# Optimization experiments

Measured on AMD Instinct MI355X. Metric: run time of the kernel, lower is better.

## Reference

```python
import jax, jax.numpy as jnp
import numpy as np

D = 128      # flattened state dim (n_dim)
T = 128      # time grid length
N = 32       # quadrature nodes per integral
H = 256      # func MLP hidden
HK = 64      # kernel MLP hidden
ITERS = 3    # IDESolver max_iterations


def setup_inputs() -> dict:
    key = jax.random.key(0)
    ks = jax.random.split(key, 6)
    z0 = jax.random.normal(ks[0], (1, D), jnp.float32)
    t = jnp.linspace(0.0, 1.0, T, dtype=jnp.float32)
    W1 = jax.random.normal(ks[1], (D, H), jnp.float32) / np.float32(np.sqrt(D))
    b1 = jnp.zeros((H,), jnp.float32)
    W2 = jax.random.normal(ks[2], (H, D), jnp.float32) / np.float32(np.sqrt(H))
    b2 = jnp.zeros((D,), jnp.float32)
    Wk1 = jax.random.normal(ks[3], (2, HK), jnp.float32) / np.float32(np.sqrt(2))
    bk1 = jnp.zeros((HK,), jnp.float32)
    # small kernel init keeps the Picard iteration stable
    Wk2 = jax.random.normal(ks[4], (HK, D * D), jnp.float32) * np.float32(0.01 / np.sqrt(HK))
    bk2 = jnp.zeros((D * D,), jnp.float32)
    return dict(z0=z0, t=t, W1=W1, b1=b1, W2=W2, b2=b2,
                Wk1=Wk1, bk1=bk1, Wk2=Wk2, bk2=bk2)


def _spline_coeffs(x, y):
    # natural cubic spline second derivatives M: tridiagonal system, natural BC
    n = x.shape[0]
    h = x[1:] - x[:-1]                       # [T-1]
    A = jnp.zeros((n, n), y.dtype).at[0, 0].set(1.0).at[n - 1, n - 1].set(1.0)
    idx = jnp.arange(1, n - 1)
    A = A.at[idx, idx - 1].set(h[:-1])
    A = A.at[idx, idx].set(2.0 * (h[:-1] + h[1:]))
    A = A.at[idx, idx + 1].set(h[1:])
    slope = (y[1:] - y[:-1]) / h[:, None]
    rhs = jnp.zeros_like(y).at[1:-1].set(6.0 * (slope[1:] - slope[:-1]))
    return jnp.linalg.solve(A, rhs)          # [T, D]


def _spline_eval(x, y, M, q):
    # evaluate spline at flat query points q [Q] -> [Q, D]
    qc = jnp.clip(q, x[0], x[-1])
    i = jnp.clip(jnp.searchsorted(x, qc, side='right') - 1, 0, x.shape[0] - 2)
    h = x[i + 1] - x[i]
    a = (x[i + 1] - qc) / h
    b = (qc - x[i]) / h
    return (a[:, None] * y[i] + b[:, None] * y[i + 1]
            + ((a ** 3 - a)[:, None] * M[i] + (b ** 3 - b)[:, None] * M[i + 1])
            * (h ** 2 / 6.0)[:, None])


def _F(y, W1, b1, W2, b2):
    return jnp.tanh(y @ W1 + b1) @ W2 + b2


def _K(ts, Wk1, bk1, Wk2, bk2):
    # ts [..., 2] -> kernel matrices [..., D, D]
    hden = jnp.tanh(ts @ Wk1 + bk1)
    return (hden @ Wk2 + bk2).reshape(ts.shape[:-1] + (D, D))


def reference(z0, t, W1, b1, W2, b2, Wk1, bk1, Wk2, bk2):
    y0 = z0.reshape(-1)                          # solver state: flattened z0 [D]
    u = jnp.linspace(0.0, 1.0, N, dtype=t.dtype) # unit quad nodes
    wq = jnp.ones((N,), t.dtype).at[0].set(0.5).at[-1].set(0.5)  # trapezoid
    mids = 0.5 * (t[:-1] + t[1:])
    xs = jnp.concatenate([t, mids])              # eval points [P = 2T-1]
    hstep = t[1:] - t[:-1]
    yg = jnp.broadcast_to(y0, (T, D))            # Picard initial guess y^(0)=y0
    for _ in range(ITERS):
        M = _spline_coeffs(t, yg)
        s = xs[:, None] * u[None, :]                              # [P, N], lb=0, ub=x
        ys = _spline_eval(t, yg, M, s.reshape(-1)).reshape(-1, N, D)
        fy = _F(ys, W1, b1, W2, b2)                               # [P, N, D]
        ts = jnp.stack([jnp.broadcast_to(xs[:, None], s.shape), s], -1)
        k = _K(ts, Wk1, bk1, Wk2, bk2)                            # [P, N, D, D]
        integ = jnp.einsum('pnij,pnj->pni', k, fy)
        g = jnp.einsum('pni,n->pi', integ, wq) * (xs / (N - 1))[:, None]  # [P, D]
        g_t, g_m = g[:T], g[T:]
        # Simpson (== RK4 for y-independent RHS) + cumulative integration
        inc = (hstep[:, None] / 6.0) * (g_t[:-1] + 4.0 * g_m + g_t[1:])
        yg = y0[None, :] + jnp.concatenate(
            [jnp.zeros((1, D), yg.dtype), jnp.cumsum(inc, axis=0)])
    return yg[:, None, :]                        # [T, 1, D] like solver.y.unsqueeze(1)
```

## Files before the change

### kernel.cpp

```cpp
#include <hip/hip_runtime.h>
#include <hip/hip_fp16.h>

#define D_  128
#define T_  128
#define P_  255
#define SROW 8320
#define GSZ  32640

#define OFF_YGT   0
#define OFF_COEF  8192
#define OFF_AINV  8704
#define OFF_G     25088
#define OFF_E     41472
#define OFF_HDW   563712
#define OFF_W1T   828912
#define OFF_W2T   845296
#define OFF_WTT   861680
#define OFF_S     1394160
#define OFF_G2    2459120

typedef _Float16 f16;
typedef _Float16 f16x4 __attribute__((ext_vector_type(4)));
typedef float f32x4 __attribute__((ext_vector_type(4)));

__device__ __forceinline__ float tanh_fast(float x) {
  float e = __expf(2.0f * x);
  return 1.0f - 2.0f / (e + 1.0f);
}

__device__ __forceinline__ f16x4 ldfrag(const f16* buf, int row, int kunits,
                                        int kk, int quad) {
  int u = row * kunits + ((kk * 4 + quad) ^ (row & 7));
  return *(const f16x4*)(buf + 4 * u);
}

__global__ __launch_bounds__(256) void k_setup(
    const float* __restrict__ z0, const float* __restrict__ tgrid,
    const float* __restrict__ W1, const float* __restrict__ W2,
    const float* __restrict__ Wk2, const float* __restrict__ bk2,
    __half* __restrict__ ygT, float* __restrict__ coef,
    float* __restrict__ Ainv, __half* __restrict__ W1T,
    __half* __restrict__ W2T, __half* __restrict__ WTT) {
  __shared__ __align__(16) unsigned char smem[66560];
  int bid = blockIdx.x, tid = threadIdx.x;
  for (int idx = bid * 256 + tid; idx < 65 * 16384; idx += 256 * 256) {
    int c = idx >> 14, rem = idx & 16383;
    int i = rem >> 7, j = rem & 127;
    float v = (c < 64) ? Wk2[idx] : bk2[rem];
    WTT[i * 8320 + c * 128 + j] = __float2half(v);
  }
  if (bid == 0) {
    for (int idx = tid; idx < 16384; idx += 256) {
      int grow = idx >> 7, d = idx & 127;
      ygT[d * 128 + grow] = __float2half(z0[d]);
    }
  } else if (bid == 1) {
    for (int idx = tid; idx < 32768; idx += 256) {
      int c = idx >> 7, d = idx & 127;
      W1T[idx] = __float2half(W1[d * 256 + c]);
    }
  } else if (bid == 2) {
    for (int idx = tid; idx < 32768; idx += 256) {
      int j = idx >> 8, c2 = idx & 255;
      W2T[idx] = __float2half(W2[c2 * 128 + j]);
    }
  } else if (bid == 255) {
    float* dpL = (float*)smem;
    float* tl  = (float*)(smem + 65024);
    float* cpL = tl + 128;
    float* imL = cpL + 128;
    if (tid < 128) tl[tid] = tgrid[tid];
    __syncthreads();
    if (tid == 0) {
      cpL[0] = 0.0f;
      float cprev = 0.0f;
      for (int i = 1; i <= 126; ++i) {
        float hm = tl[i] - tl[i - 1], hi = tl[i + 1] - tl[i];
        float m = 2.0f * (hm + hi) - hm * cprev;
        float im = 1.0f / m;
        imL[i] = im;
        cprev = hi * im;
        cpL[i] = cprev;
      }
    }
    if (tid < 127) coef[256 + tid] = 1.0f / (tl[tid + 1] - tl[tid]);
    __syncthreads();
    if (tid < 128) {
      int d = tid;
      float dprev = (d == 0) ? 1.0f : 0.0f;
      dpL[d] = dprev;
      for (int i = 1; i <= 126; ++i) {
        float rhs = (i == d) ? 1.0f : 0.0f;
        float hm = tl[i] - tl[i - 1];
        dprev = (rhs - hm * dprev) * imL[i];
        dpL[i * 128 + d] = dprev;
      }
      float x = (d == 127) ? 1.0f : 0.0f;
      Ainv[127 * 128 + d] = x;
      for (int i = 126; i >= 0; --i) {
        x = dpL[i * 128 + d] - cpL[i] * x;
        Ainv[i * 128 + d] = x;
      }
    }
  }
}

__global__ __launch_bounds__(256) void k_G(const float* __restrict__ coef,
                                           const float* __restrict__ Ainv,
                                           float* __restrict__ G) {
  int idx = blockIdx.x * 256 + threadIdx.x;
  int a = idx >> 7, b = idx & 127;
  const float* ih = coef + 256;
  float acc = 0.0f;
  if (b >= 2)             acc += Ainv[a * 128 + b - 1] * (6.0f * ih[b - 1]);
  if (b >= 1 && b <= 126) acc += Ainv[a * 128 + b] * (-6.0f * (ih[b - 1] + ih[b]));
  if (b <= 125)           acc += Ainv[a * 128 + b + 1] * (6.0f * ih[b]);
  G[idx] = acc;
}

__global__ __launch_bounds__(256) void k_EH(const float* __restrict__ t,
                                            const float* __restrict__ Wk1,
                                            const float* __restrict__ bk1,
                                            const float* __restrict__ G,
                                            __half* __restrict__ E,
                                            __half* __restrict__ HDW) {
  __shared__ float tl[128];
  __shared__ float sn[32], an[32], bn[32], cA[32], cB[32];
  __shared__ int idn[32];
  int p = blockIdx.x, tid = threadIdx.x;
  if (tid < 128) tl[tid] = t[tid];
  __syncthreads();
  float xp = (p < T_) ? tl[p] : 0.5f * (tl[p - T_] + tl[p - T_ + 1]);
  if (tid < 32) {
    int n = tid;
    float u = (float)n * (1.0f / 31.0f);
    float q = xp * u;
    float qc = fminf(fmaxf(q, tl[0]), tl[127]);
    int i = (int)floorf(qc * 127.0f);
    i = max(0, min(126, i));
    while (i > 0 && qc < tl[i]) --i;
    while (i < 126 && qc >= tl[i + 1]) ++i;
    float h = tl[i + 1] - tl[i];
    float aa = (tl[i + 1] - qc) / h, bb = (qc - tl[i]) / h;
    sn[n] = q; idn[n] = i; an[n] = aa; bn[n] = bb;
    float h26 = h * h * (1.0f / 6.0f);
    cA[n] = (aa * aa * aa - aa) * h26;
    cB[n] = (bb * bb * bb - bb) * h26;
  }
  __syncthreads();
  #pragma unroll
  for (int pass = 0; pass < 16; ++pass) {
    int n = pass * 2 + (tid >> 7);
    int b = tid & 127;
    int i = idn[n];
    float v = cA[n] * G[i * 128 + b] + cB[n] * G[(i + 1) * 128 + b];
    if (b == i) v += an[n];
    if (b == i + 1) v += bn[n];
    E[(p * 32 + n) * 128 + b] = __float2half(v);
  }
  #pragma unroll
  for (int k = 0; k < 9; ++k) {
    int idx = k * 256 + tid;
    if (idx < 2080) {
      int c = idx >> 5, n = idx & 31;
      float wq = (n == 0 || n == 31) ? 0.5f : 1.0f;
      float v = (c < 64)
          ? wq * tanh_fast(fmaf(xp, Wk1[c], fmaf(sn[n], Wk1[64 + c], bk1[c])))
          : wq;
      HDW[p * 2080 + idx] = __float2half(v);
    }
  }
}

__global__ __launch_bounds__(256) void k_fused(
    const __half* __restrict__ ygT, const __half* __restrict__ E,
    const __half* __restrict__ HDW,
    const __half* __restrict__ W1T, const __half* __restrict__ W2T,
    const float* __restrict__ b1, const float* __restrict__ b2,
    __half* __restrict__ Sh, float* __restrict__ g) {
  __shared__ __align__(16) unsigned char smem[65536];
  f16* RW = (f16*)smem;
  f16* RA = (f16*)(smem + 32768);
  f16* RB = (f16*)(smem + 40960);
  f16* RC = (f16*)(smem + 49152);
  int p = blockIdx.x, tid = threadIdx.x;
  int wv = tid >> 6, l = tid & 63, quad = l >> 4, r = l & 15;

  if (tid < 128) g[p * 128 + tid] = 0.0f;
  if (p == 0) {
    unsigned* zrow = (unsigned*)(Sh + 255 * SROW);
    for (int z = tid; z < SROW / 2; z += 256) zrow[z] = 0u;
  }

  {
    const uint2* src = (const uint2*)ygT;
    uint2* dst = (uint2*)RW;
    #pragma unroll
    for (int k = 0; k < 16; ++k) {
      int idx = k * 256 + tid;
      int row = idx >> 5, k4 = idx & 31;
      dst[row * 32 + (k4 ^ (row & 7))] = src[idx];
    }
    const uint2* se = (const uint2*)(E + p * 4096);
    uint2* da = (uint2*)RA;
    #pragma unroll
    for (int k = 0; k < 4; ++k) {
      int idx = k * 256 + tid;
      int row = idx >> 5, k4 = idx & 31;
      da[row * 32 + (k4 ^ (row & 7))] = se[idx];
    }
  }
  __syncthreads();
  for (int tt = wv; tt < 16; tt += 4) {
    int mt = tt >> 3, nt = tt & 7;
    f32x4 acc = {0.f, 0.f, 0.f, 0.f};
    #pragma unroll
    for (int kk = 0; kk < 8; ++kk) {
      f16x4 av = ldfrag(RA, mt * 16 + r, 32, kk, quad);
      f16x4 bv = ldfrag(RW, nt * 16 + r, 32, kk, quad);
      acc = __builtin_amdgcn_mfma_f32_16x16x16f16(av, bv, acc, 0, 0, 0);
    }
    int col = nt * 16 + r;
    #pragma unroll
    for (int i = 0; i < 4; ++i) {
      int row = mt * 16 + quad * 4 + i;
      RB[row * 128 + (col ^ ((row & 7) << 2))] = (f16)acc[i];
    }
  }
  for (int hf = 0; hf < 2; ++hf) {
    __syncthreads();
    {
      const uint2* src = (const uint2*)(W1T + hf * 16384);
      uint2* dst = (uint2*)RW;
      #pragma unroll
      for (int k = 0; k < 16; ++k) {
        int idx = k * 256 + tid;
        int row = idx >> 5, k4 = idx & 31;
        dst[row * 32 + (k4 ^ (row & 7))] = src[idx];
      }
    }
    __syncthreads();
    int c0 = hf * 128;
    for (int tt = wv; tt < 16; tt += 4) {
      int mt = tt >> 3, nt = tt & 7;
      f32x4 acc = {0.f, 0.f, 0.f, 0.f};
      #pragma unroll
      for (int kk = 0; kk < 8; ++kk) {
        f16x4 av = ldfrag(RB, mt * 16 + r, 32, kk, quad);
        f16x4 bv = ldfrag(RW, nt * 16 + r, 32, kk, quad);
        acc = __builtin_amdgcn_mfma_f32_16x16x16f16(av, bv, acc, 0, 0, 0);
      }
      int colg = c0 + nt * 16 + r;
      float bias = b1[colg];
      #pragma unroll
      for (int i = 0; i < 4; ++i) {
        int row = mt * 16 + quad * 4 + i;
        RC[row * 256 + (colg ^ ((row & 7) << 2))] = (f16)tanh_fast(acc[i] + bias);
      }
    }
  }
  __syncthreads();
  {
    const uint2* sh_ = (const uint2*)(HDW + p * 2080);
    uint2* db = (uint2*)RB;
    #pragma unroll
    for (int k = 0; k < 3; ++k) {
      int idx = k * 256 + tid;
      if (idx < 640) {
        int row = idx >> 3, k4 = idx & 7;
        uint2 v = (idx < 520) ? sh_[idx] : make_uint2(0u, 0u);
        db[row * 8 + (k4 ^ (row & 7))] = v;
      }
    }
    const uint2* src = (const uint2*)W2T;
    uint2* dst = (uint2*)RW;
    #pragma unroll
    for (int k = 0; k < 16; ++k) {
      int idx = k * 256 + tid;
      int row = idx >> 6, k4 = idx & 63;
      dst[row * 64 + (k4 ^ (row & 7))] = src[idx];
    }
  }
  __syncthreads();
  for (int hf = 0; hf < 2; ++hf) {
    if (hf) {
      __syncthreads();
      const uint2* src = (const uint2*)(W2T + 16384);
      uint2* dst = (uint2*)RW;
      #pragma unroll
      for (int k = 0; k < 16; ++k) {
        int idx = k * 256 + tid;
        int row = idx >> 6, k4 = idx & 63;
        dst[row * 64 + (k4 ^ (row & 7))] = src[idx];
      }
      __syncthreads();
    }
    int j0 = hf * 64;
    for (int tt = wv; tt < 8; tt += 4) {
      int mt = tt >> 2, nt = tt & 3;
      f32x4 acc = {0.f, 0.f, 0.f, 0.f};
      #pragma unroll
      for (int kk = 0; kk < 16; ++kk) {
        f16x4 av = ldfrag(RC, mt * 16 + r, 64, kk, quad);
        f16x4 bv = ldfrag(RW, nt * 16 + r, 64, kk, quad);
        acc = __builtin_amdgcn_mfma_f32_16x16x16f16(av, bv, acc, 0, 0, 0);
      }
      int jg = j0 + nt * 16 + r;
      float bias = b2[jg];
      #pragma unroll
      for (int i = 0; i < 4; ++i) {
        int n = mt * 16 + quad * 4 + i;
        RA[jg * 32 + (n ^ ((jg & 7) << 2))] = (f16)(acc[i] + bias);
      }
    }
  }
  __syncthreads();
  for (int tt = wv; tt < 40; tt += 4) {
    int mt = tt >> 3, nt = tt & 7;
    f32x4 acc = {0.f, 0.f, 0.f, 0.f};
    #pragma unroll
    for (int kk = 0; kk < 2; ++kk) {
      f16x4 av = ldfrag(RB, mt * 16 + r, 8, kk, quad);
      f16x4 bv = ldfrag(RA, nt * 16 + r, 8, kk, quad);
      acc = __builtin_amdgcn_mfma_f32_16x16x16f16(av, bv, acc, 0, 0, 0);
    }
    #pragma unroll
    for (int i = 0; i < 4; ++i) {
      int c = mt * 16 + quad * 4 + i;
      if (c < 65) Sh[p * SROW + c * 128 + nt * 16 + r] = __float2half(acc[i]);
    }
  }
}

__global__ __launch_bounds__(256) void k_gemmM(const __half* __restrict__ Sh,
                                               const __half* __restrict__ WTT,
                                               float* __restrict__ g) {
  int mt = blockIdx.x;
  int kc = blockIdx.y;
  int tid = threadIdx.x;
  int wv = tid >> 6, l = tid & 63, q = l >> 4, r = l & 15;
  int p0 = mt * 16;
  const f16* Arow = (const f16*)Sh + (p0 + r) * SROW + kc * 1040 + 4 * q;
  const f16* B0 = (const f16*)WTT + (wv * 32 + r) * 8320 + kc * 1040 + 4 * q;
  const f16* B1 = B0 + 16 * 8320;
  f32x4 acc0 = {0.f, 0.f, 0.f, 0.f}, acc1 = {0.f, 0.f, 0.f, 0.f};
  #pragma unroll 5
  for (int ks = 0; ks < 65; ++ks) {
    f16x4 av = *(const f16x4*)(Arow + ks * 16);
    f16x4 b0 = *(const f16x4*)(B0 + ks * 16);
    f16x4 b1 = *(const f16x4*)(B1 + ks * 16);
    acc0 = __builtin_amdgcn_mfma_f32_16x16x16f16(av, b0, acc0, 0, 0, 0);
    acc1 = __builtin_amdgcn_mfma_f32_16x16x16f16(av, b1, acc1, 0, 0, 0);
  }
  #pragma unroll
  for (int t = 0; t < 4; ++t) {
    int p = p0 + 4 * q + t;
    if (p < 255) {
      atomicAdd(&g[p * 128 + wv * 32 + r], acc0[t]);
      atomicAdd(&g[p * 128 + wv * 32 + 16 + r], acc1[t]);
    }
  }
}

__global__ __launch_bounds__(256) void k_final(const float* __restrict__ t,
                                               const float* __restrict__ z0,
                                               const float* __restrict__ g,
                                               __half* __restrict__ ygT,
                                               float* __restrict__ out, int wout) {
  __shared__ float incL[127 * 128];
  int tid = threadIdx.x;
  for (int idx = tid; idx < 127 * 128; idx += 256) {
    int k = idx >> 7, d = idx & 127;
    float tk = t[k], tk1 = t[k + 1];
    float h = tk1 - tk;
    float sct  = tk * (1.0f / 31.0f);
    float scm  = 0.5f * (tk + tk1) * (1.0f / 31.0f);
    float sct1 = tk1 * (1.0f / 31.0f);
    incL[idx] = h * (1.0f / 6.0f) *
        (g[k * 128 + d] * sct + 4.0f * g[(T_ + k) * 128 + d] * scm +
         g[(k + 1) * 128 + d] * sct1);
  }
  __syncthreads();
  if (tid < 128) {
    int d = tid;
    float acc = z0[d];
    ygT[d * 128] = __float2half(acc);
    if (wout) out[d] = acc;
    #pragma unroll 4
    for (int k = 0; k < 127; ++k) {
      acc += incL[k * 128 + d];
      ygT[d * 128 + k + 1] = __float2half(acc);
      if (wout) out[(k + 1) * 128 + d] = acc;
    }
  }
}

extern "C" void kernel_launch(void* const* d_in, const int* in_sizes, int n_in,
                              void* d_out, int out_size, void* d_ws, size_t ws_size,
                              hipStream_t stream) {
  const float* z0  = (const float*)d_in[0];
  const float* t   = (const float*)d_in[1];
  const float* W1  = (const float*)d_in[2];
  const float* b1  = (const float*)d_in[3];
  const float* W2  = (const float*)d_in[4];
  const float* b2  = (const float*)d_in[5];
  const float* Wk1 = (const float*)d_in[6];
  const float* bk1 = (const float*)d_in[7];
  const float* Wk2 = (const float*)d_in[8];
  const float* bk2 = (const float*)d_in[9];
  float* out = (float*)d_out;
  float* ws  = (float*)d_ws;

  __half* ygT  = (__half*)(ws + OFF_YGT);
  float*  coef = ws + OFF_COEF;
  float*  Ainv = ws + OFF_AINV;
  float*  G    = ws + OFF_G;
  __half* E    = (__half*)(ws + OFF_E);
  __half* HDW  = (__half*)(ws + OFF_HDW);
  __half* W1T  = (__half*)(ws + OFF_W1T);
  __half* W2T  = (__half*)(ws + OFF_W2T);
  __half* WTT  = (__half*)(ws + OFF_WTT);
  __half* Sh   = (__half*)(ws + OFF_S);
  float*  g    = ws + OFF_G2;

  k_setup<<<dim3(256), dim3(256), 0, stream>>>(z0, t, W1, W2, Wk2, bk2,
                                               ygT, coef, Ainv, W1T, W2T, WTT);
  k_G<<<dim3(64), dim3(256), 0, stream>>>(coef, Ainv, G);
  k_EH<<<dim3(255), dim3(256), 0, stream>>>(t, Wk1, bk1, G, E, HDW);
  for (int it = 0; it < 3; ++it) {
    k_fused<<<dim3(255), dim3(256), 0, stream>>>(ygT, E, HDW, W1T, W2T,
                                                 b1, b2, Sh, g);
    k_gemmM<<<dim3(16, 8), dim3(256), 0, stream>>>(Sh, WTT, g);
    k_final<<<dim3(1), dim3(256), 0, stream>>>(t, z0, g, ygT, out,
                                               (it == 2) ? 1 : 0);
  }
}
```

Measured before the change: 208.7 us.

## Fuse k_G into k_EH, fold k_final into gemmM via last-block counter, widen k_fused

```diff
diff --git a/kernel.cpp b/kernel.cpp
--- a/kernel.cpp
+++ b/kernel.cpp
@@ -18,6 +18,7 @@
 #define OFF_WTT   861680
 #define OFF_S     1394160
 #define OFF_G2    2459120
+#define OFF_CTR   2491760
 
 typedef _Float16 f16;
 typedef _Float16 f16x4 __attribute__((ext_vector_type(4)));
@@ -40,7 +41,8 @@
     const float* __restrict__ Wk2, const float* __restrict__ bk2,
     __half* __restrict__ ygT, float* __restrict__ coef,
     float* __restrict__ Ainv, __half* __restrict__ W1T,
-    __half* __restrict__ W2T, __half* __restrict__ WTT) {
+    __half* __restrict__ W2T, __half* __restrict__ WTT,
+    unsigned* __restrict__ ctr) {
   __shared__ __align__(16) unsigned char smem[66560];
   int bid = blockIdx.x, tid = threadIdx.x;
   for (int idx = bid * 256 + tid; idx < 65 * 16384; idx += 256 * 256) {
@@ -64,6 +66,8 @@
       int j = idx >> 8, c2 = idx & 255;
       W2T[idx] = __float2half(W2[c2 * 128 + j]);
     }
+  } else if (bid == 3) {
+    if (tid == 0) *ctr = 0u;
   } else if (bid == 255) {
     float* dpL = (float*)smem;
     float* tl  = (float*)(smem + 65024);
@@ -105,30 +109,19 @@
   }
 }
 
-__global__ __launch_bounds__(256) void k_G(const float* __restrict__ coef,
-                                           const float* __restrict__ Ainv,
-                                           float* __restrict__ G) {
-  int idx = blockIdx.x * 256 + threadIdx.x;
-  int a = idx >> 7, b = idx & 127;
-  const float* ih = coef + 256;
-  float acc = 0.0f;
-  if (b >= 2)             acc += Ainv[a * 128 + b - 1] * (6.0f * ih[b - 1]);
-  if (b >= 1 && b <= 126) acc += Ainv[a * 128 + b] * (-6.0f * (ih[b - 1] + ih[b]));
-  if (b <= 125)           acc += Ainv[a * 128 + b + 1] * (6.0f * ih[b]);
-  G[idx] = acc;
-}
-
 __global__ __launch_bounds__(256) void k_EH(const float* __restrict__ t,
                                             const float* __restrict__ Wk1,
                                             const float* __restrict__ bk1,
-                                            const float* __restrict__ G,
+                                            const float* __restrict__ coef,
+                                            const float* __restrict__ Ainv,
                                             __half* __restrict__ E,
                                             __half* __restrict__ HDW) {
-  __shared__ float tl[128];
+  __shared__ float tl[128], ihL[128];
   __shared__ float sn[32], an[32], bn[32], cA[32], cB[32];
   __shared__ int idn[32];
   int p = blockIdx.x, tid = threadIdx.x;
   if (tid < 128) tl[tid] = t[tid];
+  if (tid < 127) ihL[tid] = coef[256 + tid];
   __syncthreads();
   float xp = (p < T_) ? tl[p] : 0.5f * (tl[p - T_] + tl[p - T_ + 1]);
   if (tid < 32) {
@@ -153,7 +146,23 @@
     int n = pass * 2 + (tid >> 7);
     int b = tid & 127;
     int i = idn[n];
-    float v = cA[n] * G[i * 128 + b] + cB[n] * G[(i + 1) * 128 + b];
+    float Gi = 0.0f, Gi1 = 0.0f;
+    if (b >= 2) {
+      float w = 6.0f * ihL[b - 1];
+      Gi  += Ainv[i * 128 + b - 1] * w;
+      Gi1 += Ainv[(i + 1) * 128 + b - 1] * w;
+    }
+    if (b >= 1 && b <= 126) {
+      float w = -6.0f * (ihL[b - 1] + ihL[b]);
+      Gi  += Ainv[i * 128 + b] * w;
+      Gi1 += Ainv[(i + 1) * 128 + b] * w;
+    }
+    if (b <= 125) {
+      float w = 6.0f * ihL[b];
+      Gi  += Ainv[i * 128 + b + 1] * w;
+      Gi1 += Ainv[(i + 1) * 128 + b + 1] * w;
+    }
+    float v = cA[n] * Gi + cB[n] * Gi1;
     if (b == i) v += an[n];
     if (b == i + 1) v += bn[n];
     E[(p * 32 + n) * 128 + b] = __float2half(v);
@@ -172,7 +181,7 @@
   }
 }
 
-__global__ __launch_bounds__(256) void k_fused(
+__global__ __launch_bounds__(512) void k_fused(
     const __half* __restrict__ ygT, const __half* __restrict__ E,
     const __half* __restrict__ HDW,
     const __half* __restrict__ W1T, const __half* __restrict__ W2T,
@@ -189,29 +198,29 @@
   if (tid < 128) g[p * 128 + tid] = 0.0f;
   if (p == 0) {
     unsigned* zrow = (unsigned*)(Sh + 255 * SROW);
-    for (int z = tid; z < SROW / 2; z += 256) zrow[z] = 0u;
+    for (int z = tid; z < SROW / 2; z += 512) zrow[z] = 0u;
   }
 
   {
     const uint2* src = (const uint2*)ygT;
     uint2* dst = (uint2*)RW;
     #pragma unroll
-    for (int k = 0; k < 16; ++k) {
-      int idx = k * 256 + tid;
+    for (int k = 0; k < 8; ++k) {
+      int idx = k * 512 + tid;
       int row = idx >> 5, k4 = idx & 31;
       dst[row * 32 + (k4 ^ (row & 7))] = src[idx];
     }
     const uint2* se = (const uint2*)(E + p * 4096);
     uint2* da = (uint2*)RA;
     #pragma unroll
-    for (int k = 0; k < 4; ++k) {
-      int idx = k * 256 + tid;
+    for (int k = 0; k < 2; ++k) {
+      int idx = k * 512 + tid;
       int row = idx >> 5, k4 = idx & 31;
       da[row * 32 + (k4 ^ (row & 7))] = se[idx];
     }
   }
   __syncthreads();
-  for (int tt = wv; tt < 16; tt += 4) {
+  for (int tt = wv; tt < 16; tt += 8) {
     int mt = tt >> 3, nt = tt & 7;
     f32x4 acc = {0.f, 0.f, 0.f, 0.f};
     #pragma unroll
@@ -233,15 +242,15 @@
       const uint2* src = (const uint2*)(W1T + hf * 16384);
       uint2* dst = (uint2*)RW;
       #pragma unroll
-      for (int k = 0; k < 16; ++k) {
-        int idx = k * 256 + tid;
+      for (int k = 0; k < 8; ++k) {
+        int idx = k * 512 + tid;
         int row = idx >> 5, k4 = idx & 31;
         dst[row * 32 + (k4 ^ (row & 7))] = src[idx];
       }
     }
     __syncthreads();
     int c0 = hf * 128;
-    for (int tt = wv; tt < 16; tt += 4) {
+    for (int tt = wv; tt < 16; tt += 8) {
       int mt = tt >> 3, nt = tt & 7;
       f32x4 acc = {0.f, 0.f, 0.f, 0.f};
       #pragma unroll
@@ -264,8 +273,8 @@
     const uint2* sh_ = (const uint2*)(HDW + p * 2080);
     uint2* db = (uint2*)RB;
     #pragma unroll
-    for (int k = 0; k < 3; ++k) {
-      int idx = k * 256 + tid;
+    for (int k = 0; k < 2; ++k) {
+      int idx = k * 512 + tid;
       if (idx < 640) {
         int row = idx >> 3, k4 = idx & 7;
         uint2 v = (idx < 520) ? sh_[idx] : make_uint2(0u, 0u);
@@ -275,8 +284,8 @@
     const uint2* src = (const uint2*)W2T;
     uint2* dst = (uint2*)RW;
     #pragma unroll
-    for (int k = 0; k < 16; ++k) {
-      int idx = k * 256 + tid;
+    for (int k = 0; k < 8; ++k) {
+      int idx = k * 512 + tid;
       int row = idx >> 6, k4 = idx & 63;
       dst[row * 64 + (k4 ^ (row & 7))] = src[idx];
     }
@@ -288,15 +297,15 @@
       const uint2* src = (const uint2*)(W2T + 16384);
       uint2* dst = (uint2*)RW;
       #pragma unroll
-      for (int k = 0; k < 16; ++k) {
-        int idx = k * 256 + tid;
+      for (int k = 0; k < 8; ++k) {
+        int idx = k * 512 + tid;
         int row = idx >> 6, k4 = idx & 63;
         dst[row * 64 + (k4 ^ (row & 7))] = src[idx];
       }
       __syncthreads();
     }
     int j0 = hf * 64;
-    for (int tt = wv; tt < 8; tt += 4) {
+    for (int tt = wv; tt < 8; tt += 8) {
       int mt = tt >> 2, nt = tt & 3;
       f32x4 acc = {0.f, 0.f, 0.f, 0.f};
       #pragma unroll
@@ -315,7 +324,7 @@
     }
   }
   __syncthreads();
-  for (int tt = wv; tt < 40; tt += 4) {
+  for (int tt = wv; tt < 40; tt += 8) {
     int mt = tt >> 3, nt = tt & 7;
     f32x4 acc = {0.f, 0.f, 0.f, 0.f};
     #pragma unroll
@@ -332,9 +341,13 @@
   }
 }
 
-__global__ __launch_bounds__(256) void k_gemmM(const __half* __restrict__ Sh,
-                                               const __half* __restrict__ WTT,
-                                               float* __restrict__ g) {
+__global__ __launch_bounds__(256) void k_gemmM(
+    const __half* __restrict__ Sh, const __half* __restrict__ WTT,
+    float* __restrict__ g, const float* __restrict__ t,
+    const float* __restrict__ z0, __half* __restrict__ ygT,
+    float* __restrict__ out, unsigned* __restrict__ ctr, int wout) {
+  __shared__ float incL[127 * 128];
+  __shared__ unsigned lastFlag;
   int mt = blockIdx.x;
   int kc = blockIdx.y;
   int tid = threadIdx.x;
@@ -353,22 +366,22 @@
     acc1 = __builtin_amdgcn_mfma_f32_16x16x16f16(av, b1, acc1, 0, 0, 0);
   }
   #pragma unroll
-  for (int t = 0; t < 4; ++t) {
-    int p = p0 + 4 * q + t;
+  for (int tt = 0; tt < 4; ++tt) {
+    int p = p0 + 4 * q + tt;
     if (p < 255) {
-      atomicAdd(&g[p * 128 + wv * 32 + r], acc0[t]);
-      atomicAdd(&g[p * 128 + wv * 32 + 16 + r], acc1[t]);
-    }
-  }
-}
-
-__global__ __launch_bounds__(256) void k_final(const float* __restrict__ t,
-                                               const float* __restrict__ z0,
-                                               const float* __restrict__ g,
-                                               __half* __restrict__ ygT,
-                                               float* __restrict__ out, int wout) {
-  __shared__ float incL[127 * 128];
-  int tid = threadIdx.x;
+      atomicAdd(&g[p * 128 + wv * 32 + r], acc0[tt]);
+      atomicAdd(&g[p * 128 + wv * 32 + 16 + r], acc1[tt]);
+    }
+  }
+  __threadfence();
+  if (tid == 0) {
+    unsigned old = atomicAdd(ctr, 1u);
+    lastFlag = (old == 127u) ? 1u : 0u;
+    if (lastFlag) *ctr = 0u;
+  }
+  __syncthreads();
+  if (!lastFlag) return;
+  __threadfence();
   for (int idx = tid; idx < 127 * 128; idx += 256) {
     int k = idx >> 7, d = idx & 127;
     float tk = t[k], tk1 = t[k + 1];
@@ -411,27 +424,26 @@
   float* out = (float*)d_out;
   float* ws  = (float*)d_ws;
 
-  __half* ygT  = (__half*)(ws + OFF_YGT);
-  float*  coef = ws + OFF_COEF;
-  float*  Ainv = ws + OFF_AINV;
-  float*  G    = ws + OFF_G;
-  __half* E    = (__half*)(ws + OFF_E);
-  __half* HDW  = (__half*)(ws + OFF_HDW);
-  __half* W1T  = (__half*)(ws + OFF_W1T);
-  __half* W2T  = (__half*)(ws + OFF_W2T);
-  __half* WTT  = (__half*)(ws + OFF_WTT);
-  __half* Sh   = (__half*)(ws + OFF_S);
-  float*  g    = ws + OFF_G2;
+  __half*   ygT  = (__half*)(ws + OFF_YGT);
+  float*    coef = ws + OFF_COEF;
+  float*    Ainv = ws + OFF_AINV;
+  __half*   E    = (__half*)(ws + OFF_E);
+  __half*   HDW  = (__half*)(ws + OFF_HDW);
+  __half*   W1T  = (__half*)(ws + OFF_W1T);
+  __half*   W2T  = (__half*)(ws + OFF_W2T);
+  __half*   WTT  = (__half*)(ws + OFF_WTT);
+  __half*   Sh   = (__half*)(ws + OFF_S);
+  float*    g    = ws + OFF_G2;
+  unsigned* ctr  = (unsigned*)(ws + OFF_CTR);
 
   k_setup<<<dim3(256), dim3(256), 0, stream>>>(z0, t, W1, W2, Wk2, bk2,
-                                               ygT, coef, Ainv, W1T, W2T, WTT);
-  k_G<<<dim3(64), dim3(256), 0, stream>>>(coef, Ainv, G);
-  k_EH<<<dim3(255), dim3(256), 0, stream>>>(t, Wk1, bk1, G, E, HDW);
+                                               ygT, coef, Ainv, W1T, W2T, WTT,
+                                               ctr);
+  k_EH<<<dim3(255), dim3(256), 0, stream>>>(t, Wk1, bk1, coef, Ainv, E, HDW);
   for (int it = 0; it < 3; ++it) {
-    k_fused<<<dim3(255), dim3(256), 0, stream>>>(ygT, E, HDW, W1T, W2T,
+    k_fused<<<dim3(255), dim3(512), 0, stream>>>(ygT, E, HDW, W1T, W2T,
                                                  b1, b2, Sh, g);
-    k_gemmM<<<dim3(16, 8), dim3(256), 0, stream>>>(Sh, WTT, g);
-    k_final<<<dim3(1), dim3(256), 0, stream>>>(t, z0, g, ygT, out,
-                                               (it == 2) ? 1 : 0);
-  }
-}
+    k_gemmM<<<dim3(16, 8), dim3(256), 0, stream>>>(Sh, WTT, g, t, z0, ygT, out,
+                                                   ctr, (it == 2) ? 1 : 0);
+  }
+}
```

Measured after the change: 216.1 us. 1.04x slower.
